# Performance work log

Measured on AMD Instinct MI355X. Metric: run time of the kernel, lower is better.

Reference implementation:

```python
import jax, jax.numpy as jnp
import numpy as np

EMBED_DIM = 1024
HEADS = 16
HD = EMBED_DIM // HEADS

def setup_inputs() -> dict:
    key = jax.random.key(0)
    ks = jax.random.split(key, 6)
    s = 1.0 / np.sqrt(EMBED_DIM)
    x = jax.random.normal(ks[0], (4, 2048, EMBED_DIM), dtype=jnp.float32)
    Wq = jax.random.uniform(ks[1], (EMBED_DIM, EMBED_DIM), jnp.float32, -s, s)
    Wk = jax.random.uniform(ks[2], (EMBED_DIM, EMBED_DIM), jnp.float32, -s, s)
    Wv = jax.random.uniform(ks[3], (EMBED_DIM, EMBED_DIM), jnp.float32, -s, s)
    Wo = jax.random.uniform(ks[4], (EMBED_DIM, EMBED_DIM), jnp.float32, -s, s)
    bo = jax.random.uniform(ks[5], (EMBED_DIM,), jnp.float32, -s, s)
    return {"x": x, "Wq": Wq, "Wk": Wk, "Wv": Wv, "Wo": Wo, "bo": bo}

def reference(x, Wq, Wk, Wv, Wo, bo):
    B, S, E = x.shape
    # projections (torch Linear: y = x @ W.T), split into heads -> [B,H,S,hd]
    def proj(W):
        return (x @ W.T).reshape(B, S, HEADS, HD).transpose(0, 2, 1, 3)
    q, k, v = proj(Wq), proj(Wk), proj(Wv)
    energy = jnp.einsum('bhid,bhjd->bhij', q, k) / np.sqrt(HD).astype(np.float32)
    causal = jnp.tril(jnp.ones((S, S), dtype=bool))
    energy = jnp.where(causal, energy, -jnp.inf)
    attn = jax.nn.softmax(energy, axis=-1)  # dropout omitted (eval mode)
    out = jnp.einsum('bhij,bhjd->bhid', attn, v)
    out = out.transpose(0, 2, 1, 3).reshape(B, S, E)
    return out @ Wo.T + bo
```

## Files before the change

### kernel.cpp

```cpp
#include <hip/hip_runtime.h>
#include <math.h>

#define EMB   1024
#define HEADS 16
#define HD    64
#define SEQ   2048
#define BATCH 4
#define MTOT  (BATCH * SEQ)
#define XSZ   ((size_t)MTOT * EMB)
#define WSZ   ((size_t)EMB * EMB)

typedef __attribute__((ext_vector_type(8))) short s16x8;
typedef __attribute__((ext_vector_type(4))) short s16x4;
typedef __attribute__((ext_vector_type(4))) float f32x4;

__device__ __forceinline__ short f2bf(float f) {
    unsigned u = __builtin_bit_cast(unsigned, f);
    u += 0x7fffu + ((u >> 16) & 1u);
    return (short)(u >> 16);
}

__device__ __forceinline__ unsigned pk_bf16(float a, float b) {
#if __has_builtin(__builtin_amdgcn_cvt_pk_bf16_f32)
    typedef __attribute__((ext_vector_type(2))) __bf16 bf16x2;
    return __builtin_bit_cast(unsigned, __builtin_amdgcn_cvt_pk_bf16_f32(a, b));
#else
    return (unsigned)(unsigned short)f2bf(a) |
           ((unsigned)(unsigned short)f2bf(b) << 16);
#endif
}

__device__ __forceinline__ float fexp2(float x) {
#if __has_builtin(__builtin_amdgcn_exp2f)
    return __builtin_amdgcn_exp2f(x);
#else
    return exp2f(x);
#endif
}

__device__ __forceinline__ void async16(const void* g, void* l) {
    __builtin_amdgcn_global_load_lds(
        (const __attribute__((address_space(1))) unsigned*)g,
        (__attribute__((address_space(3))) unsigned*)l, 16, 0, 0);
}

__global__ __launch_bounds__(256)
void cvt_inputs(const float* __restrict__ x,  const float* __restrict__ wq,
                const float* __restrict__ wk, const float* __restrict__ wv,
                const float* __restrict__ wo, short* __restrict__ xb,
                short* __restrict__ wcat)
{
    const size_t e = ((size_t)blockIdx.x * 256 + threadIdx.x) * 8;
    const float* src;
    short* dst;
    float scale = 1.0f;
    if (e < XSZ) {
        src = x + e;
        dst = xb + e;
    } else {
        const size_t r = e - XSZ;
        const int w = (int)(r >> 20);
        const size_t off = r & (WSZ - 1);
        src = (w == 0 ? wq : w == 1 ? wk : w == 2 ? wv : wo) + off;
        dst = wcat + r;
        if (w == 0) scale = 0.125f * 1.44269504f;
    }
    const float4 a = ((const float4*)src)[0];
    const float4 b = ((const float4*)src)[1];
    s16x8 v;
    v[0] = f2bf(a.x * scale); v[1] = f2bf(a.y * scale);
    v[2] = f2bf(a.z * scale); v[3] = f2bf(a.w * scale);
    v[4] = f2bf(b.x * scale); v[5] = f2bf(b.y * scale);
    v[6] = f2bf(b.z * scale); v[7] = f2bf(b.w * scale);
    *(s16x8*)dst = v;
}

#define BAR() __builtin_amdgcn_s_barrier()
#define WAIT_LGKM() do { asm volatile("s_waitcnt lgkmcnt(0)" ::: "memory"); \
                         __builtin_amdgcn_sched_barrier(0); } while (0)
#define WAIT_VM(n) asm volatile("s_waitcnt vmcnt(" #n ")" ::: "memory")

#define STG32(dst, k0) do { \
    async16(pA32 + (k0),                     (dst) + wv1024); \
    async16(pA32 + (size_t)128 * EMB + (k0), (dst) + 8192 + wv1024); \
    async16(pB32 + (k0),                     (dst) + 16384 + wv1024); \
} while (0)

__global__ __launch_bounds__(512, 2)
void gemm_qkv32(const short* __restrict__ A, const short* __restrict__ B,
                short* __restrict__ C, int ldc, short* __restrict__ Vt)
{
    __shared__ __align__(16) char lds[49152];

    const int tid   = threadIdx.x;
    const int wv    = tid >> 6;
    const int lane  = tid & 63;
    const int col16 = lane & 15;
    const int quad  = lane >> 4;
    const int wm    = wv >> 1;
    const int wn    = wv & 1;
    const int wm4   = wm * 4;
    const int wn4   = wn * 4;
    const int wv1024 = wv << 10;

    const int nwg = gridDim.x * gridDim.y;
    int wg = blockIdx.y * gridDim.x + blockIdx.x;
    wg = (wg & 7) * (nwg >> 3) + (wg >> 3);
    const int rowBase = (wg / gridDim.x) * 256;
    const int colBase = (wg % gridDim.x) * 128;

    const int abase = (col16 * 64 + quad * 16) ^ ((col16 & 8) << 2);

    const int rlane = (lane >> 2) & 15;
    const int colSt = ((lane & 3) << 3) ^ ((lane & 32) >> 1);
    const short* pA32 = A + (size_t)(rowBase + wv * 16 + rlane) * EMB + colSt;
    const short* pB32 = B + (size_t)(colBase + wv * 16 + rlane) * EMB + colSt;

    s16x8 a[4], bq[4];
    f32x4 acc[4][4];
#pragma unroll
    for (int i = 0; i < 4; ++i)
#pragma unroll
        for (int j = 0; j < 4; ++j) acc[i][j] = (f32x4){0.f, 0.f, 0.f, 0.f};

    char* cb = lds;
    char* nb = lds + 24576;

    STG32(cb, 0);

    for (int kt = 0; kt < 32; ++kt) {
        const int k0 = kt << 5;
        const bool more = (kt + 1 < 32);

        if (more) STG32(nb, k0 + 32);
        if (more) { WAIT_VM(3); } else { WAIT_VM(0); }
        BAR();

#pragma unroll
        for (int mi = 0; mi < 4; ++mi)
            a[mi] = *(const s16x8*)(cb + (wm4 + mi) * 1024 + abase);
#pragma unroll
        for (int ni = 0; ni < 4; ++ni)
            bq[ni] = *(const s16x8*)(cb + 16384 + (wn4 + ni) * 1024 + abase);
        WAIT_LGKM();

        __builtin_amdgcn_s_setprio(1);
#pragma unroll
        for (int mi = 0; mi < 4; ++mi)
#pragma unroll
            for (int ni = 0; ni < 4; ++ni)
                acc[mi][ni] = __builtin_amdgcn_mfma_f32_16x16x32_bf16(
                    a[mi], bq[ni], acc[mi][ni], 0, 0, 0);
        __builtin_amdgcn_s_setprio(0);
        BAR();

        char* t = cb; cb = nb; nb = t;
    }

    if (colBase >= 2048) {
#pragma unroll
        for (int mi = 0; mi < 4; ++mi) {
            const int rg0 = rowBase + wm * 64 + mi * 16 + quad * 4;
            const int bq_ = rg0 >> 11;
            const int s0 = rg0 & 2047;
#pragma unroll
            for (int ni = 0; ni < 4; ++ni) {
                const int cg2 = colBase - 2048 + wn * 64 + ni * 16 + col16;
                const int hh = cg2 >> 6, dd = cg2 & 63;
                short* dst = Vt + (((size_t)(bq_ * 16 + hh) * 64 + dd) << 11) + s0;
                const f32x4 v = acc[mi][ni];
                uint2 pw;
                pw.x = pk_bf16(v[0], v[1]);
                pw.y = pk_bf16(v[2], v[3]);
                *(uint2*)dst = pw;
            }
        }
    } else {
#pragma unroll
        for (int mi = 0; mi < 4; ++mi) {
            const int rg0 = rowBase + wm * 64 + mi * 16 + quad * 4;
#pragma unroll
            for (int ni = 0; ni < 4; ++ni) {
                const int cg = colBase + wn * 64 + ni * 16 + col16;
                const f32x4 v = acc[mi][ni];
#pragma unroll
                for (int r = 0; r < 4; ++r)
                    C[(size_t)(rg0 + r) * ldc + cg] = f2bf(v[r]);
            }
        }
    }
}

#define RD_A4(bA) \
    _Pragma("unroll") for (int mi = 0; mi < 4; ++mi) \
    _Pragma("unroll") for (int kk = 0; kk < 2; ++kk) \
        a[mi][kk] = *(const s16x8*)((bA) + (wm4 + mi) * 2048 + kk * 1024 + abase);

#define RD_B2(bB, hf, breg) \
    _Pragma("unroll") for (int ni = 0; ni < 2; ++ni) \
    _Pragma("unroll") for (int kk = 0; kk < 2; ++kk) \
        breg[ni][kk] = *(const s16x8*)((bB) + (wn4 + (hf) * 2 + ni) * 2048 + kk * 1024 + abase);

#define MFMA16(hf, breg) \
    __builtin_amdgcn_s_setprio(1); \
    _Pragma("unroll") for (int mi = 0; mi < 4; ++mi) \
    _Pragma("unroll") for (int ni = 0; ni < 2; ++ni) \
    _Pragma("unroll") for (int kk = 0; kk < 2; ++kk) \
        acc[mi][(hf) * 2 + ni] = __builtin_amdgcn_mfma_f32_16x16x32_bf16( \
            a[mi][kk], breg[ni][kk], acc[mi][(hf) * 2 + ni], 0, 0, 0); \
    __builtin_amdgcn_s_setprio(0);

#define STA(pM, ldsM, h, k0) do { \
    async16((pM) + (size_t)((h) * 128) * K + (k0),      (ldsM) + (h) * 16384 + wv1024); \
    async16((pM) + (size_t)((h) * 128 + 64) * K + (k0), (ldsM) + (h) * 16384 + 8192 + wv1024); \
} while (0)

#define STB(pM, ldsM, k0) do { \
    async16((pM) + (k0),                (ldsM) + wv1024); \
    async16((pM) + (size_t)64 * K + (k0), (ldsM) + 8192 + wv1024); \
} while (0)

__global__ __launch_bounds__(512, 2)
void gemm_out(const short* __restrict__ A, const short* __restrict__ B,
              float* __restrict__ C, int ldc, const float* __restrict__ bias,
              int K)
{
    __shared__ __align__(16) char lds[147456];

    const int tid   = threadIdx.x;
    const int wv    = tid >> 6;
    const int lane  = tid & 63;
    const int col16 = lane & 15;
    const int quad  = lane >> 4;
    const int wm    = wv >> 1;
    const int wn    = wv & 1;
    const int wm4   = wm * 4;
    const int wn4   = wn * 4;
    const int wv1024 = wv << 10;

    const int nwg = gridDim.x * gridDim.y;
    int wg = blockIdx.y * gridDim.x + blockIdx.x;
    wg = (wg & 7) * (nwg >> 3) + (wg >> 3);
    const int rowBase = (wg / gridDim.x) * 256;
    const int colBase = (wg % gridDim.x) * 128;

    const int abase = (col16 * 64 + quad * 16) ^ ((col16 & 8) << 2);

    const int rlane = (lane >> 2) & 15;
    const int rw0   = ((wv >> 1) << 4) + rlane;
    const int colSt = ((wv & 1) << 5) + (((lane & 3) << 3) ^ ((lane & 32) >> 1));
    const short* pA = A + (size_t)(rowBase + rw0) * K + colSt;
    const short* pB = B + (size_t)(colBase + rw0) * K + colSt;

    s16x8 a[4][2], bq0[2][2], bq1[2][2];
    f32x4 acc[4][4];
#pragma unroll
    for (int i = 0; i < 4; ++i)
#pragma unroll
        for (int j = 0; j < 4; ++j) acc[i][j] = (f32x4){0.f, 0.f, 0.f, 0.f};

    const int NT = K >> 6;

    char* r0 = lds;
    char* r1 = lds + 49152;
    char* r2 = lds + 98304;

    STA(pA, r0, 0, 0);  STA(pA, r0, 1, 0);  STB(pB, r0 + 32768, 0);
    STA(pA, r1, 0, 64); STA(pA, r1, 1, 64); STB(pB, r1 + 32768, 64);
    WAIT_VM(6);
    BAR();

    for (int kt = 0; kt < NT; ++kt) {
        const int k0 = kt << 6;
        const bool more = (kt + 2 < NT);

        RD_A4(r0);
        RD_B2(r0 + 32768, 0, bq0);
        if (more) { STA(pA, r2, 0, k0 + 128); STB(pB, r2 + 32768, k0 + 128); }
        BAR(); WAIT_LGKM();
        MFMA16(0, bq0);
        BAR();

        RD_B2(r0 + 32768, 1, bq1);
        if (more) STA(pA, r2, 1, k0 + 128);
        BAR(); WAIT_LGKM();
        MFMA16(1, bq1);
        if (more) { WAIT_VM(6); } else { WAIT_VM(0); }
        BAR();

        char* t = r0; r0 = r1; r1 = r2; r2 = t;
    }

#pragma unroll
    for (int ni = 0; ni < 4; ++ni) {
        const int cg = colBase + wn * 64 + ni * 16 + col16;
        const float bj = bias ? bias[cg] : 0.f;
#pragma unroll
        for (int mi = 0; mi < 4; ++mi) {
            const int rg0 = rowBase + wm * 64 + mi * 16 + quad * 4;
            const f32x4 v = acc[mi][ni];
#pragma unroll
            for (int r = 0; r < 4; ++r)
                C[(size_t)(rg0 + r) * ldc + cg] = v[r] + bj;
        }
    }
}

#define LDT 2048
__global__ __launch_bounds__(512)
void attn_mfma(const short* __restrict__ QK, const short* __restrict__ VT,
               short* __restrict__ O)
{
    __shared__ __align__(16) short lKV[3][2][64 * 64];
    __shared__ __align__(16) short lP[8 * 16 * 64];

    char* lPc = (char*)lP;

    const int tid  = threadIdx.x;
    const int wv   = tid >> 6;
    const int lane = tid & 63;
    const int col  = lane & 15;
    const int quad = lane >> 4;
    const int csw  = (col & 7) << 4;

    const int qpair = (int)blockIdx.x;
    const int bh = blockIdx.y;
    const int b  = bh >> 4;
    const int h  = bh & 15;
    const size_t baseq = (size_t)b * SEQ * LDT + (size_t)h * HD;
    const size_t basek = baseq + 1024;
    const size_t baseo = (size_t)b * SEQ * EMB + (size_t)h * HD;
    const short* vtb = VT + ((size_t)bh << 17);

    const int srow   = tid >> 3;
    const int schunk = tid & 7;
    const int ssc    = (schunk ^ (srow & 7)) * 8;
    const int sdst   = srow * 128 + schunk * 16;

    char* pwv = lPc + wv * 2048;

    const s16x8 onesv = {0x3F80, 0x3F80, 0x3F80, 0x3F80,
                         0x3F80, 0x3F80, 0x3F80, 0x3F80};

#define STG(kt, bp) do { \
    async16(QK + basek + (size_t)((kt) * 64 + srow) * LDT + ssc, (char*)((bp)[0]) + sdst); \
    async16(vtb + (size_t)srow * LDT + (kt) * 64 + ssc,          (char*)((bp)[1]) + sdst); \
} while (0)

    for (int half = 0; half < 2; ++half) {
        const int qx = half ? (15 - qpair) : qpair;
        const int qb = qx * 128;
        const int qlo_w = qb + wv * 16;

        s16x8 qf[2];
        {
            const short* qr = QK + baseq + (size_t)(qlo_w + col) * LDT;
            qf[0] = *(const s16x8*)(qr + quad * 8);
            qf[1] = *(const s16x8*)(qr + 32 + quad * 8);
        }

        f32x4 of[4], lsum;
#pragma unroll
        for (int u = 0; u < 4; ++u) of[u] = (f32x4){0.f, 0.f, 0.f, 0.f};
        lsum = (f32x4){0.f, 0.f, 0.f, 0.f};

        const int nt = qb / 64 + 2;

        short (*b0)[64 * 64] = lKV[0];
        short (*b1)[64 * 64] = lKV[1];
        short (*b2)[64 * 64] = lKV[2];

        BAR();
        __builtin_amdgcn_sched_barrier(0);
        STG(0, b0);
        STG(1, b1);

        for (int kt = 0; kt < nt; ++kt) {
            const int kb = kt * 64;
            if (kt + 1 < nt) { WAIT_VM(2); } else { WAIT_VM(0); }
            BAR();
            __builtin_amdgcn_sched_barrier(0);
            if (kt + 2 < nt) STG(kt + 2, b2);

            if (kb <= qlo_w + 15) {
                const char* lKb = (const char*)(b0[0]);
                const char* lVb = (const char*)(b0[1]);

                s16x8 kf[4][2];
#pragma unroll
                for (int t = 0; t < 4; ++t) {
                    kf[t][0] = *(const s16x8*)(lKb + (t * 16 + col) * 128 + ((quad * 16) ^ csw));
                    kf[t][1] = *(const s16x8*)(lKb + (t * 16 + col) * 128 + ((64 + quad * 16) ^ csw));
                }

                f32x4 s[4];
#pragma unroll
                for (int t = 0; t < 4; ++t) {
                    f32x4 acc = (f32x4){0.f, 0.f, 0.f, 0.f};
                    acc = __builtin_amdgcn_mfma_f32_16x16x32_bf16(kf[t][0], qf[0], acc, 0, 0, 0);
                    acc = __builtin_amdgcn_mfma_f32_16x16x32_bf16(kf[t][1], qf[1], acc, 0, 0, 0);
                    s[t] = acc;
                }

                const int qg = qlo_w + col;
                if (kb + 63 > qlo_w) {
#pragma unroll
                    for (int t = 0; t < 4; ++t)
#pragma unroll
                        for (int rr = 0; rr < 4; ++rr) {
                            const int kg = kb + t * 16 + quad * 4 + rr;
                            if (kg > qg) s[t][rr] = -3.0e38f;
                        }
                }

                char* pb = pwv + col * 128;
#pragma unroll
                for (int t = 0; t < 4; ++t) {
                    uint2 pkd;
                    pkd.x = pk_bf16(fexp2(s[t][0]), fexp2(s[t][1]));
                    pkd.y = pk_bf16(fexp2(s[t][2]), fexp2(s[t][3]));
                    *(uint2*)(pb + ((t * 32 + quad * 8) ^ csw)) = pkd;
                }

#pragma unroll
                for (int c = 0; c < 2; ++c) {
                    s16x8 vf[4];
#pragma unroll
                    for (int u = 0; u < 4; ++u)
                        vf[u] = *(const s16x8*)(lVb + (u * 16 + col) * 128 + ((c * 64 + quad * 16) ^ csw));
                    const s16x8 pa = *(const s16x8*)(pwv + col * 128 + ((c * 64 + quad * 16) ^ csw));
                    lsum = __builtin_amdgcn_mfma_f32_16x16x32_bf16(onesv, pa, lsum, 0, 0, 0);
#pragma unroll
                    for (int u = 0; u < 4; ++u)
                        of[u] = __builtin_amdgcn_mfma_f32_16x16x32_bf16(vf[u], pa, of[u], 0, 0, 0);
                }
            }

            short (*tmp)[64 * 64] = b0; b0 = b1; b1 = b2; b2 = tmp;
        }

        const float rl = 1.f / lsum[0];
        short* orow = O + baseo + (size_t)(qlo_w + col) * EMB + quad * 4;
#pragma unroll
        for (int u = 0; u < 4; ++u) {
            uint2 pkd;
            pkd.x = pk_bf16(of[u][0] * rl, of[u][1] * rl);
            pkd.y = pk_bf16(of[u][2] * rl, of[u][3] * rl);
            *(uint2*)&orow[u * 16] = pkd;
        }
    }
#undef STG
}

extern "C" void kernel_launch(void* const* d_in, const int* in_sizes, int n_in,
                              void* d_out, int out_size, void* d_ws, size_t ws_size,
                              hipStream_t stream)
{
    const float* x  = (const float*)d_in[0];
    const float* Wq = (const float*)d_in[1];
    const float* Wk = (const float*)d_in[2];
    const float* Wv = (const float*)d_in[3];
    const float* Wo = (const float*)d_in[4];
    const float* bo = (const float*)d_in[5];
    float* out = (float*)d_out;

    short* xb   = (short*)d_ws;
    short* wcat = xb + XSZ;
    short* qk   = wcat + 4 * WSZ;
    short* vt   = qk + (size_t)MTOT * 2048;
    short* ob   = vt + (size_t)64 * 64 * 2048;

    const int cvt_blocks = (int)((XSZ + 4 * WSZ) / 8 / 256);
    cvt_inputs<<<cvt_blocks, 256, 0, stream>>>(x, Wq, Wk, Wv, Wo, xb, wcat);

    gemm_qkv32<<<dim3(3072 / 128, MTOT / 256), 512, 0, stream>>>(
        xb, wcat, qk, 2048, vt);

    attn_mfma<<<dim3(8, BATCH * HEADS), 512, 0, stream>>>(qk, vt, ob);

    gemm_out<<<dim3(EMB / 128, MTOT / 256), 512, 0, stream>>>(
        ob, wcat + (size_t)3 * WSZ, out, EMB, bo, EMB);
}
```

Baseline: 230.3 us.

## Triple-buffer the K32 GEMM pipeline and reuse it for the output projection

Turns the QKV projection GEMM into a template with a three-stage LDS ring. Each iteration now waits on the oldest stage and uses one barrier instead of two, then issues the next prefetch two stages ahead. The separate K64 output-projection GEMM with its 144 KB LDS buffer is removed, and the output projection now uses the same template with a float-plus-bias epilogue. This is meant to cut barrier stalls and hide load latency better. In exchange, QKV uses more LDS per block (72 KB instead of 48 KB), and the output GEMM moves to a different pipeline shape that may perform differently.

```diff
diff --git a/kernel.cpp b/kernel.cpp
--- a/kernel.cpp
+++ b/kernel.cpp
@@ -86,11 +86,13 @@
     async16(pB32 + (k0),                     (dst) + 16384 + wv1024); \
 } while (0)
 
+template<bool QKV>
 __global__ __launch_bounds__(512, 2)
-void gemm_qkv32(const short* __restrict__ A, const short* __restrict__ B,
-                short* __restrict__ C, int ldc, short* __restrict__ Vt)
+void gemm_p32(const short* __restrict__ A, const short* __restrict__ B,
+              void* __restrict__ C, int ldc, const float* __restrict__ bias,
+              short* __restrict__ Vt)
 {
-    __shared__ __align__(16) char lds[49152];
+    __shared__ __align__(16) char lds[73728];
 
     const int tid   = threadIdx.x;
     const int wv    = tid >> 6;
@@ -123,25 +125,27 @@
 #pragma unroll
         for (int j = 0; j < 4; ++j) acc[i][j] = (f32x4){0.f, 0.f, 0.f, 0.f};
 
-    char* cb = lds;
-    char* nb = lds + 24576;
-
-    STG32(cb, 0);
+    char* b0 = lds;
+    char* b1 = lds + 24576;
+    char* b2 = lds + 49152;
+
+    STG32(b0, 0);
+    STG32(b1, 32);
 
     for (int kt = 0; kt < 32; ++kt) {
         const int k0 = kt << 5;
-        const bool more = (kt + 1 < 32);
-
-        if (more) STG32(nb, k0 + 32);
-        if (more) { WAIT_VM(3); } else { WAIT_VM(0); }
+
+        if (kt + 1 < 32) { WAIT_VM(3); } else { WAIT_VM(0); }
         BAR();
+        __builtin_amdgcn_sched_barrier(0);
+        if (kt + 2 < 32) STG32(b2, k0 + 64);
 
 #pragma unroll
         for (int mi = 0; mi < 4; ++mi)
-            a[mi] = *(const s16x8*)(cb + (wm4 + mi) * 1024 + abase);
+            a[mi] = *(const s16x8*)(b0 + (wm4 + mi) * 1024 + abase);
 #pragma unroll
         for (int ni = 0; ni < 4; ++ni)
-            bq[ni] = *(const s16x8*)(cb + 16384 + (wn4 + ni) * 1024 + abase);
+            bq[ni] = *(const s16x8*)(b0 + 16384 + (wn4 + ni) * 1024 + abase);
         WAIT_LGKM();
 
         __builtin_amdgcn_s_setprio(1);
@@ -152,156 +156,58 @@
                 acc[mi][ni] = __builtin_amdgcn_mfma_f32_16x16x32_bf16(
                     a[mi], bq[ni], acc[mi][ni], 0, 0, 0);
         __builtin_amdgcn_s_setprio(0);
-        BAR();
-
-        char* t = cb; cb = nb; nb = t;
+
+        char* t = b0; b0 = b1; b1 = b2; b2 = t;
     }
 
-    if (colBase >= 2048) {
-#pragma unroll
-        for (int mi = 0; mi < 4; ++mi) {
-            const int rg0 = rowBase + wm * 64 + mi * 16 + quad * 4;
-            const int bq_ = rg0 >> 11;
-            const int s0 = rg0 & 2047;
-#pragma unroll
-            for (int ni = 0; ni < 4; ++ni) {
-                const int cg2 = colBase - 2048 + wn * 64 + ni * 16 + col16;
-                const int hh = cg2 >> 6, dd = cg2 & 63;
-                short* dst = Vt + (((size_t)(bq_ * 16 + hh) * 64 + dd) << 11) + s0;
+    if (QKV) {
+        short* Cb = (short*)C;
+        if (colBase >= 2048) {
+#pragma unroll
+            for (int mi = 0; mi < 4; ++mi) {
+                const int rg0 = rowBase + wm * 64 + mi * 16 + quad * 4;
+                const int bq_ = rg0 >> 11;
+                const int s0 = rg0 & 2047;
+#pragma unroll
+                for (int ni = 0; ni < 4; ++ni) {
+                    const int cg2 = colBase - 2048 + wn * 64 + ni * 16 + col16;
+                    const int hh = cg2 >> 6, dd = cg2 & 63;
+                    short* dst = Vt + (((size_t)(bq_ * 16 + hh) * 64 + dd) << 11) + s0;
+                    const f32x4 v = acc[mi][ni];
+                    uint2 pw;
+                    pw.x = pk_bf16(v[0], v[1]);
+                    pw.y = pk_bf16(v[2], v[3]);
+                    *(uint2*)dst = pw;
+                }
+            }
+        } else {
+#pragma unroll
+            for (int mi = 0; mi < 4; ++mi) {
+                const int rg0 = rowBase + wm * 64 + mi * 16 + quad * 4;
+#pragma unroll
+                for (int ni = 0; ni < 4; ++ni) {
+                    const int cg = colBase + wn * 64 + ni * 16 + col16;
+                    const f32x4 v = acc[mi][ni];
+#pragma unroll
+                    for (int r = 0; r < 4; ++r)
+                        Cb[(size_t)(rg0 + r) * ldc + cg] = f2bf(v[r]);
+                }
+            }
+        }
+    } else {
+        float* Cf = (float*)C;
+#pragma unroll
+        for (int ni = 0; ni < 4; ++ni) {
+            const int cg = colBase + wn * 64 + ni * 16 + col16;
+            const float bj = bias ? bias[cg] : 0.f;
+#pragma unroll
+            for (int mi = 0; mi < 4; ++mi) {
+                const int rg0 = rowBase + wm * 64 + mi * 16 + quad * 4;
                 const f32x4 v = acc[mi][ni];
-                uint2 pw;
-                pw.x = pk_bf16(v[0], v[1]);
-                pw.y = pk_bf16(v[2], v[3]);
-                *(uint2*)dst = pw;
+#pragma unroll
+                for (int r = 0; r < 4; ++r)
+                    Cf[(size_t)(rg0 + r) * ldc + cg] = v[r] + bj;
             }
-        }
-    } else {
-#pragma unroll
-        for (int mi = 0; mi < 4; ++mi) {
-            const int rg0 = rowBase + wm * 64 + mi * 16 + quad * 4;
-#pragma unroll
-            for (int ni = 0; ni < 4; ++ni) {
-                const int cg = colBase + wn * 64 + ni * 16 + col16;
-                const f32x4 v = acc[mi][ni];
-#pragma unroll
-                for (int r = 0; r < 4; ++r)
-                    C[(size_t)(rg0 + r) * ldc + cg] = f2bf(v[r]);
-            }
-        }
-    }
-}
-
-#define RD_A4(bA) \
-    _Pragma("unroll") for (int mi = 0; mi < 4; ++mi) \
-    _Pragma("unroll") for (int kk = 0; kk < 2; ++kk) \
-        a[mi][kk] = *(const s16x8*)((bA) + (wm4 + mi) * 2048 + kk * 1024 + abase);
-
-#define RD_B2(bB, hf, breg) \
-    _Pragma("unroll") for (int ni = 0; ni < 2; ++ni) \
-    _Pragma("unroll") for (int kk = 0; kk < 2; ++kk) \
-        breg[ni][kk] = *(const s16x8*)((bB) + (wn4 + (hf) * 2 + ni) * 2048 + kk * 1024 + abase);
-
-#define MFMA16(hf, breg) \
-    __builtin_amdgcn_s_setprio(1); \
-    _Pragma("unroll") for (int mi = 0; mi < 4; ++mi) \
-    _Pragma("unroll") for (int ni = 0; ni < 2; ++ni) \
-    _Pragma("unroll") for (int kk = 0; kk < 2; ++kk) \
-        acc[mi][(hf) * 2 + ni] = __builtin_amdgcn_mfma_f32_16x16x32_bf16( \
-            a[mi][kk], breg[ni][kk], acc[mi][(hf) * 2 + ni], 0, 0, 0); \
-    __builtin_amdgcn_s_setprio(0);
-
-#define STA(pM, ldsM, h, k0) do { \
-    async16((pM) + (size_t)((h) * 128) * K + (k0),      (ldsM) + (h) * 16384 + wv1024); \
-    async16((pM) + (size_t)((h) * 128 + 64) * K + (k0), (ldsM) + (h) * 16384 + 8192 + wv1024); \
-} while (0)
-
-#define STB(pM, ldsM, k0) do { \
-    async16((pM) + (k0),                (ldsM) + wv1024); \
-    async16((pM) + (size_t)64 * K + (k0), (ldsM) + 8192 + wv1024); \
-} while (0)
-
-__global__ __launch_bounds__(512, 2)
-void gemm_out(const short* __restrict__ A, const short* __restrict__ B,
-              float* __restrict__ C, int ldc, const float* __restrict__ bias,
-              int K)
-{
-    __shared__ __align__(16) char lds[147456];
-
-    const int tid   = threadIdx.x;
-    const int wv    = tid >> 6;
-    const int lane  = tid & 63;
-    const int col16 = lane & 15;
-    const int quad  = lane >> 4;
-    const int wm    = wv >> 1;
-    const int wn    = wv & 1;
-    const int wm4   = wm * 4;
-    const int wn4   = wn * 4;
-    const int wv1024 = wv << 10;
-
-    const int nwg = gridDim.x * gridDim.y;
-    int wg = blockIdx.y * gridDim.x + blockIdx.x;
-    wg = (wg & 7) * (nwg >> 3) + (wg >> 3);
-    const int rowBase = (wg / gridDim.x) * 256;
-    const int colBase = (wg % gridDim.x) * 128;
-
-    const int abase = (col16 * 64 + quad * 16) ^ ((col16 & 8) << 2);
-
-    const int rlane = (lane >> 2) & 15;
-    const int rw0   = ((wv >> 1) << 4) + rlane;
-    const int colSt = ((wv & 1) << 5) + (((lane & 3) << 3) ^ ((lane & 32) >> 1));
-    const short* pA = A + (size_t)(rowBase + rw0) * K + colSt;
-    const short* pB = B + (size_t)(colBase + rw0) * K + colSt;
-
-    s16x8 a[4][2], bq0[2][2], bq1[2][2];
-    f32x4 acc[4][4];
-#pragma unroll
-    for (int i = 0; i < 4; ++i)
-#pragma unroll
-        for (int j = 0; j < 4; ++j) acc[i][j] = (f32x4){0.f, 0.f, 0.f, 0.f};
-
-    const int NT = K >> 6;
-
-    char* r0 = lds;
-    char* r1 = lds + 49152;
-    char* r2 = lds + 98304;
-
-    STA(pA, r0, 0, 0);  STA(pA, r0, 1, 0);  STB(pB, r0 + 32768, 0);
-    STA(pA, r1, 0, 64); STA(pA, r1, 1, 64); STB(pB, r1 + 32768, 64);
-    WAIT_VM(6);
-    BAR();
-
-    for (int kt = 0; kt < NT; ++kt) {
-        const int k0 = kt << 6;
-        const bool more = (kt + 2 < NT);
-
-        RD_A4(r0);
-        RD_B2(r0 + 32768, 0, bq0);
-        if (more) { STA(pA, r2, 0, k0 + 128); STB(pB, r2 + 32768, k0 + 128); }
-        BAR(); WAIT_LGKM();
-        MFMA16(0, bq0);
-        BAR();
-
-        RD_B2(r0 + 32768, 1, bq1);
-        if (more) STA(pA, r2, 1, k0 + 128);
-        BAR(); WAIT_LGKM();
-        MFMA16(1, bq1);
-        if (more) { WAIT_VM(6); } else { WAIT_VM(0); }
-        BAR();
-
-        char* t = r0; r0 = r1; r1 = r2; r2 = t;
-    }
-
-#pragma unroll
-    for (int ni = 0; ni < 4; ++ni) {
-        const int cg = colBase + wn * 64 + ni * 16 + col16;
-        const float bj = bias ? bias[cg] : 0.f;
-#pragma unroll
-        for (int mi = 0; mi < 4; ++mi) {
-            const int rg0 = rowBase + wm * 64 + mi * 16 + quad * 4;
-            const f32x4 v = acc[mi][ni];
-#pragma unroll
-            for (int r = 0; r < 4; ++r)
-                C[(size_t)(rg0 + r) * ldc + cg] = v[r] + bj;
         }
     }
 }
@@ -473,11 +379,11 @@
     const int cvt_blocks = (int)((XSZ + 4 * WSZ) / 8 / 256);
     cvt_inputs<<<cvt_blocks, 256, 0, stream>>>(x, Wq, Wk, Wv, Wo, xb, wcat);
 
-    gemm_qkv32<<<dim3(3072 / 128, MTOT / 256), 512, 0, stream>>>(
-        xb, wcat, qk, 2048, vt);
+    gemm_p32<true><<<dim3(3072 / 128, MTOT / 256), 512, 0, stream>>>(
+        xb, wcat, qk, 2048, nullptr, vt);
 
     attn_mfma<<<dim3(8, BATCH * HEADS), 512, 0, stream>>>(qk, vt, ob);
 
-    gemm_out<<<dim3(EMB / 128, MTOT / 256), 512, 0, stream>>>(
-        ob, wcat + (size_t)3 * WSZ, out, EMB, bo, EMB);
-}
+    gemm_p32<false><<<dim3(EMB / 128, MTOT / 256), 512, 0, stream>>>(
+        ob, wcat + (size_t)3 * WSZ, out, EMB, bo, nullptr);
+}
```

Result: no change. 234.5 us (+1.8%).
